# Kernel optimization log

Hardware: AMD Instinct MI355X
Metric: run time of the kernel (lower is better)

## Reference

```python
import jax, jax.numpy as jnp
import numpy as np

PATCH = 16  # patch_size

def _patchify(images, p=PATCH):
    # images: [B, H, W] -> patches: [B, N, p*p] in raster order
    B, H, W = images.shape
    x = images.reshape(B, H // p, p, W // p, p)
    x = x.transpose(0, 1, 3, 2, 4)  # [B, H/p, W/p, p, p]
    return x.reshape(B, (H // p) * (W // p), p * p)

def setup_inputs() -> dict:
    key = jax.random.key(0)
    k1, k2 = jax.random.split(key)
    images = jax.random.normal(k1, (64, 256, 256), dtype=jnp.float32)
    vocab = jax.random.normal(k2, (4096, 256), dtype=jnp.float32)  # [V, patch^2]
    return {"images": images, "vocab": vocab}

def reference(images, vocab):
    # forward_patches: patchify (raster ordering -> identity permutation)
    patches = _patchify(images)  # [B, N, D]
    # forward_tokens: torch.cdist + argmin. argmin of Euclidean distance
    # equals argmin of squared distance; expand ||x-v||^2 to avoid the
    # explicit [B, N, V, D] difference tensor.
    v2 = jnp.sum(vocab * vocab, axis=-1)                      # [V]
    xv = jnp.einsum('bnd,vd->bnv', patches, vocab)            # [B, N, V]
    x2 = jnp.sum(patches * patches, axis=-1, keepdims=True)   # [B, N, 1]
    d2 = x2 - 2.0 * xv + v2                                   # [B, N, V]
    tokens = jnp.argmin(d2, axis=-1)                          # [B, N] int
    return patches, tokens
```

## Files before the change

kernel.cpp:

```cpp
#include <hip/hip_runtime.h>
#include <math.h>

#define PS      16
#define D       256
#define V       4096
#define M       16384
#define NSPLIT  64
#define PAIR_CAP 1048576
#define QMARGIN 130

typedef _Float16 half8 __attribute__((ext_vector_type(8)));
typedef _Float16 half4 __attribute__((ext_vector_type(4)));
typedef float    f32x4 __attribute__((ext_vector_type(4)));

__device__ __forceinline__ void gload_lds16(const void* g, void* l) {
  __builtin_amdgcn_global_load_lds(
      (const __attribute__((address_space(1))) unsigned int*)g,
      (__attribute__((address_space(3))) unsigned int*)l, 16, 0, 0);
}


__global__ __launch_bounds__(256) void prep_kernel(
    const float* __restrict__ img, const float* __restrict__ vocab,
    float* __restrict__ outp, _Float16* __restrict__ Ah2,
    _Float16* __restrict__ Vh2, float* __restrict__ v2,
    int* __restrict__ paircount) {
  if (blockIdx.x < 4096) {
    if (blockIdx.x == 0 && threadIdx.x == 0) *paircount = 0;
    const int t  = blockIdx.x * 256 + threadIdx.x;
    const int o4 = t << 2;
    const int m   = o4 >> 8;
    const int d   = o4 & 255;
    const int b   = m >> 8;
    const int n   = m & 255;
    const int py = n >> 4, px = n & 15, i = d >> 4, j = d & 15;
    const float4 v = *(const float4*)(img + (b << 16) + ((py * PS + i) << 8) + px * PS + j);
    *(float4*)(outp + o4) = v;
    half4 h = { (_Float16)v.x, (_Float16)v.y, (_Float16)v.z, (_Float16)v.w };
    const int fa = (m >> 6) * 16384 + (d >> 5) * 2048 + ((m >> 4) & 3) * 512 +
                   ((d >> 3) & 3) * 128 + (m & 15) * 8 + (d & 7);
    *(half4*)(Ah2 + fa) = h;
  } else {
    const int gtid = (blockIdx.x - 4096) * 256 + threadIdx.x;
    const int c    = gtid >> 6;
    const int lane = gtid & 63;
    const int d0   = lane << 2;
    const float4 v = *(const float4*)(vocab + (size_t)c * D + d0);
    half4 h = { (_Float16)v.x, (_Float16)v.y, (_Float16)v.z, (_Float16)v.w };
    const int fv = (c >> 8) * 65536 + (d0 >> 5) * 8192 + ((c >> 4) & 15) * 512 +
                   ((d0 >> 3) & 3) * 128 + (c & 15) * 8 + (d0 & 7);
    *(half4*)(Vh2 + fv) = h;
    float s = v.x * v.x + v.y * v.y + v.z * v.z + v.w * v.w;
    #pragma unroll
    for (int off = 32; off > 0; off >>= 1) s += __shfl_down(s, off);
    if (lane == 0) v2[c] = s;
  }
}

__global__ __launch_bounds__(256, 4) void gemm_score_kernel(
    const _Float16* __restrict__ Ah2,
    const _Float16* __restrict__ Vh2,
    const float* __restrict__ v2,
    unsigned* __restrict__ pk1, unsigned* __restrict__ pk2) {
  __shared__ __align__(16) _Float16 Af[8 * 64 * 32];

  const int tid  = threadIdx.x;
  const int lane = tid & 63;
  const int wid  = tid >> 6;
  const int rowblk = blockIdx.x;
  const int sp     = blockIdx.y;
  const int row0 = rowblk * 64;
  const int col0 = sp * 256 + wid * 64;
  const int grp  = sp * 4 + wid;

  {
    const _Float16* src = Ah2 + (size_t)rowblk * 16384 + wid * 4096 + lane * 8;
    _Float16* dst = Af + wid * 4096;
    #pragma unroll
    for (int t = 0; t < 8; ++t)
      gload_lds16(src + t * 512, dst + t * 512);
  }
  __syncthreads();

  const int cl = lane & 15;
  const int q  = lane >> 4;
  const _Float16* Ak = Af + q * 128 + cl * 8;
  const _Float16* Bk = Vh2 + (size_t)sp * 65536 + wid * 2048 + q * 128 + cl * 8;

  f32x4 acc[4][4];
  #pragma unroll
  for (int i = 0; i < 4; ++i)
    #pragma unroll
    for (int j = 0; j < 4; ++j) acc[i][j] = (f32x4){0.f, 0.f, 0.f, 0.f};

  #pragma unroll 1
  for (int kt = 0; kt < 8; ++kt) {
    half8 av[4], bp[4];
    #pragma unroll
    for (int i = 0; i < 4; ++i) av[i] = *(const half8*)(Bk + i * 512);
    #pragma unroll
    for (int j = 0; j < 4; ++j) bp[j] = *(const half8*)(Ak + j * 512);
    Bk += 8192; Ak += 2048;
    #pragma unroll
    for (int i = 0; i < 4; ++i)
      #pragma unroll
      for (int j = 0; j < 4; ++j)
        acc[i][j] = __builtin_amdgcn_mfma_f32_16x16x32_f16(av[i], bp[j], acc[i][j], 0, 0, 0);
  }

  float Cv[16];
  #pragma unroll
  for (int i = 0; i < 4; ++i) {
    const float4 vq = *(const float4*)(v2 + col0 + i * 16 + q * 4);
    #pragma unroll
    for (int r = 0; r < 4; ++r) Cv[i * 4 + r] = fmaf(vq[r], 512.0f, 524288.0f);
  }
  #pragma unroll
  for (int j = 0; j < 4; ++j) {
    unsigned K1 = 0xFFFFFFFFu, K2 = 0xFFFFFFFFu;
    #pragma unroll
    for (int i = 0; i < 4; ++i)
      #pragma unroll
      for (int r = 0; r < 4; ++r) {
        const unsigned key =
            ((unsigned)fmaf(-1024.0f, acc[i][j][r], Cv[i * 4 + r]) << 12) |
            (unsigned)(col0 + i * 16 + q * 4 + r);
        K2 = min(K2, max(K1, key));
        K1 = min(K1, key);
      }
    #pragma unroll
    for (int mask = 16; mask <= 32; mask <<= 1) {
      const unsigned o1 = (unsigned)__shfl_xor((int)K1, mask);
      const unsigned o2 = (unsigned)__shfl_xor((int)K2, mask);
      K2 = min(min(K2, o2), max(K1, o1));
      K1 = min(K1, o1);
    }
    if (q == 0) {
      pk1[(size_t)grp * M + row0 + j * 16 + cl] = K1;
      pk2[(size_t)grp * M + row0 + j * 16 + cl] = K2;
    }
  }
}

__global__ __launch_bounds__(256) void reduce_gather_kernel(
    const unsigned* __restrict__ pk1, const unsigned* __restrict__ pk2,
    float* __restrict__ tok, unsigned long long* __restrict__ minkey,
    unsigned* __restrict__ pairs, int* __restrict__ paircount) {
  const int m = blockIdx.x * 256 + threadIdx.x;
  unsigned K1 = 0xFFFFFFFFu, K2 = 0xFFFFFFFFu;
  for (int s = 0; s < NSPLIT; ++s) {
    const unsigned b1 = pk1[(size_t)s * M + m];
    const unsigned b2 = pk2[(size_t)s * M + m];
    K2 = min(min(K2, b2), max(K1, b1));
    K1 = min(K1, b1);
  }
  tok[m] = (float)(K1 & 4095u);
  minkey[m] = 0xFFFFFFFFFFFFFFFFull;
  if ((int)(K2 >> 12) - (int)(K1 >> 12) <= QMARGIN) {
    const int th = (int)(K1 >> 12) + QMARGIN;
    int cnt = 0;
    for (int s = 0; s < NSPLIT; ++s) {
      const unsigned b1 = pk1[(size_t)s * M + m];
      const unsigned b2 = pk2[(size_t)s * M + m];
      cnt += ((int)(b2 >> 12) <= th) ? 64
           : (((int)(b1 >> 12) <= th) ? 1 : 0);
    }
    int base = atomicAdd(paircount, cnt);
    if (base + cnt <= PAIR_CAP) {
      const unsigned mh = (unsigned)m << 12;
      for (int s = 0; s < NSPLIT; ++s) {
        const unsigned b1 = pk1[(size_t)s * M + m];
        const unsigned b2 = pk2[(size_t)s * M + m];
        if ((int)(b2 >> 12) <= th) {
          for (int r = 0; r < 64; ++r) pairs[base + r] = mh | (unsigned)(s * 64 + r);
          base += 64;
        } else if ((int)(b1 >> 12) <= th) {
          pairs[base++] = mh | (b1 & 4095u);
        }
      }
    }
  }
}

__global__ __launch_bounds__(256) void refine_score(
    const float* __restrict__ patches, const float* __restrict__ vocab,
    const unsigned* __restrict__ pairs, const int* __restrict__ paircount,
    unsigned long long* __restrict__ minkey) {
  const int lane = threadIdx.x & 63;
  const int gw = (blockIdx.x * 256 + threadIdx.x) >> 6;
  const int nw = (gridDim.x * 256) >> 6;
  int np = *paircount;
  if (np > PAIR_CAP) np = PAIR_CAP;
  for (int i = gw; i < np; i += nw) {
    const unsigned pr = pairs[i];
    const int m = pr >> 12, row = pr & 4095;
    const float4 pv = *(const float4*)(patches + (size_t)m * D + (lane << 2));
    const float4 vv = *(const float4*)(vocab + (size_t)row * D + (lane << 2));
    double acc = 0.0, df;
    df = (double)pv.x - (double)vv.x; acc = fma(df, df, acc);
    df = (double)pv.y - (double)vv.y; acc = fma(df, df, acc);
    df = (double)pv.z - (double)vv.z; acc = fma(df, df, acc);
    df = (double)pv.w - (double)vv.w; acc = fma(df, df, acc);
    #pragma unroll
    for (int off = 32; off > 0; off >>= 1) acc += __shfl_down(acc, off);
    if (lane == 0) {
      const unsigned long long key =
          ((unsigned long long)__double_as_longlong(acc) & ~0xFFFull) | (unsigned)row;
      atomicMin(&minkey[m], key);
    }
  }
}

__global__ __launch_bounds__(256) void refine_final(
    const unsigned* __restrict__ pairs, const int* __restrict__ paircount,
    const unsigned long long* __restrict__ minkey, float* __restrict__ tok) {
  int np = *paircount;
  if (np > PAIR_CAP) np = PAIR_CAP;
  for (int i = blockIdx.x * 256 + threadIdx.x; i < np; i += gridDim.x * 256) {
    const int m = pairs[i] >> 12;
    tok[m] = (float)(unsigned)(minkey[m] & 4095ull);
  }
}

extern "C" void kernel_launch(void* const* d_in, const int* in_sizes, int n_in,
                              void* d_out, int out_size, void* d_ws, size_t ws_size,
                              hipStream_t stream) {
  const float* images = (const float*)d_in[0];
  const float* vocab  = (const float*)d_in[1];
  float* out     = (float*)d_out;
  float* patches = out;
  float* tokens  = out + (size_t)M * D;

  char* ws = (char*)d_ws;
  _Float16* Ah2      = (_Float16*)(ws);
  _Float16* Vh2      = (_Float16*)(ws + 8388608);
  float*    v2       = (float*)   (ws + 10485760);
  unsigned* pk1      = (unsigned*)(ws + 10502144);
  unsigned* pk2      = (unsigned*)(ws + 14696448);
  unsigned long long* minkey = (unsigned long long*)(ws + 18890752);
  int*      paircount= (int*)     (ws + 19021824);
  unsigned* pairs    = (unsigned*)(ws + 19021888);

  prep_kernel<<<4096 + 1024, 256, 0, stream>>>(images, vocab, patches, Ah2,
                                               Vh2, v2, paircount);
  gemm_score_kernel<<<dim3(M / 64, V / 256), 256, 0, stream>>>(Ah2, Vh2, v2, pk1, pk2);
  reduce_gather_kernel<<<M / 256, 256, 0, stream>>>(pk1, pk2, tokens, minkey,
                                                    pairs, paircount);
  refine_score<<<256, 256, 0, stream>>>(patches, vocab, pairs, paircount, minkey);
  refine_final<<<32, 256, 0, stream>>>(pairs, paircount, minkey, tokens);
}
```

Before: 175.0 us.

## Shrink GEMM column tile, swap grid order, merge wave top-2 in LDS, parallelize reduce

The GEMM block now covers 128 vocab columns (32 per wave) instead of 256, with a grid whose fast axis is the column split. Pairs of waves merge their top-2 keys through LDS before writing, which keeps 64 split groups. Occupancy rises from 4 to 5 blocks per SIMD, and the reduce kernel splits the 64-way scan across 4 waves followed by an LDS merge. Each A tile is loaded from LDS twice as often relative to the compute, and the extra syncs add overhead. The refine kernels also get larger grids.

```diff
diff --git a/kernel.cpp b/kernel.cpp
--- a/kernel.cpp
+++ b/kernel.cpp
@@ -57,7 +57,7 @@
   }
 }
 
-__global__ __launch_bounds__(256, 4) void gemm_score_kernel(
+__global__ __launch_bounds__(256, 5) void gemm_score_kernel(
     const _Float16* __restrict__ Ah2,
     const _Float16* __restrict__ Vh2,
     const float* __restrict__ v2,
@@ -67,11 +67,10 @@
   const int tid  = threadIdx.x;
   const int lane = tid & 63;
   const int wid  = tid >> 6;
-  const int rowblk = blockIdx.x;
-  const int sp     = blockIdx.y;
+  const int sp     = blockIdx.x;
+  const int rowblk = blockIdx.y;
   const int row0 = rowblk * 64;
-  const int col0 = sp * 256 + wid * 64;
-  const int grp  = sp * 4 + wid;
+  const int c0w  = sp * 128 + wid * 32;
 
   {
     const _Float16* src = Ah2 + (size_t)rowblk * 16384 + wid * 4096 + lane * 8;
@@ -85,46 +84,48 @@
   const int cl = lane & 15;
   const int q  = lane >> 4;
   const _Float16* Ak = Af + q * 128 + cl * 8;
-  const _Float16* Bk = Vh2 + (size_t)sp * 65536 + wid * 2048 + q * 128 + cl * 8;
-
-  f32x4 acc[4][4];
+  const _Float16* Bk = Vh2 + (c0w >> 8) * 65536 + ((c0w >> 4) & 15) * 512 +
+                       q * 128 + cl * 8;
+
+  f32x4 acc[2][4];
   #pragma unroll
-  for (int i = 0; i < 4; ++i)
+  for (int i = 0; i < 2; ++i)
     #pragma unroll
     for (int j = 0; j < 4; ++j) acc[i][j] = (f32x4){0.f, 0.f, 0.f, 0.f};
 
   #pragma unroll 1
   for (int kt = 0; kt < 8; ++kt) {
-    half8 av[4], bp[4];
-    #pragma unroll
-    for (int i = 0; i < 4; ++i) av[i] = *(const half8*)(Bk + i * 512);
+    half8 av[2], bp[4];
+    #pragma unroll
+    for (int i = 0; i < 2; ++i) av[i] = *(const half8*)(Bk + i * 512);
     #pragma unroll
     for (int j = 0; j < 4; ++j) bp[j] = *(const half8*)(Ak + j * 512);
     Bk += 8192; Ak += 2048;
     #pragma unroll
-    for (int i = 0; i < 4; ++i)
+    for (int i = 0; i < 2; ++i)
       #pragma unroll
       for (int j = 0; j < 4; ++j)
         acc[i][j] = __builtin_amdgcn_mfma_f32_16x16x32_f16(av[i], bp[j], acc[i][j], 0, 0, 0);
   }
 
-  float Cv[16];
+  float Cv[8];
   #pragma unroll
-  for (int i = 0; i < 4; ++i) {
-    const float4 vq = *(const float4*)(v2 + col0 + i * 16 + q * 4);
+  for (int i = 0; i < 2; ++i) {
+    const float4 vq = *(const float4*)(v2 + c0w + i * 16 + q * 4);
     #pragma unroll
     for (int r = 0; r < 4; ++r) Cv[i * 4 + r] = fmaf(vq[r], 512.0f, 524288.0f);
   }
+  unsigned wk1[4], wk2[4];
   #pragma unroll
   for (int j = 0; j < 4; ++j) {
     unsigned K1 = 0xFFFFFFFFu, K2 = 0xFFFFFFFFu;
     #pragma unroll
-    for (int i = 0; i < 4; ++i)
+    for (int i = 0; i < 2; ++i)
       #pragma unroll
       for (int r = 0; r < 4; ++r) {
         const unsigned key =
             ((unsigned)fmaf(-1024.0f, acc[i][j][r], Cv[i * 4 + r]) << 12) |
-            (unsigned)(col0 + i * 16 + q * 4 + r);
+            (unsigned)(c0w + i * 16 + q * 4 + r);
         K2 = min(K2, max(K1, key));
         K1 = min(K1, key);
       }
@@ -135,10 +136,27 @@
       K2 = min(min(K2, o2), max(K1, o1));
       K1 = min(K1, o1);
     }
-    if (q == 0) {
-      pk1[(size_t)grp * M + row0 + j * 16 + cl] = K1;
-      pk2[(size_t)grp * M + row0 + j * 16 + cl] = K2;
-    }
+    wk1[j] = K1; wk2[j] = K2;
+  }
+  __syncthreads();
+  unsigned* scr = (unsigned*)Af;
+  if (q == 0) {
+    #pragma unroll
+    for (int j = 0; j < 4; ++j) {
+      const int idx = (wid >> 1) * 256 + (wid & 1) * 128 + (j * 16 + cl) * 2;
+      scr[idx] = wk1[j]; scr[idx + 1] = wk2[j];
+    }
+  }
+  __syncthreads();
+  if (tid < 128) {
+    const int pair = tid >> 6, row = tid & 63;
+    const unsigned a1 = scr[pair * 256 + row * 2], a2 = scr[pair * 256 + row * 2 + 1];
+    const unsigned b1 = scr[pair * 256 + 128 + row * 2], b2 = scr[pair * 256 + 128 + row * 2 + 1];
+    const unsigned K2 = min(min(a2, b2), max(a1, b1));
+    const unsigned K1 = min(a1, b1);
+    const int grp = sp * 2 + pair;
+    pk1[(size_t)grp * M + row0 + row] = K1;
+    pk2[(size_t)grp * M + row0 + row] = K2;
   }
 }
 
@@ -146,36 +164,51 @@
     const unsigned* __restrict__ pk1, const unsigned* __restrict__ pk2,
     float* __restrict__ tok, unsigned long long* __restrict__ minkey,
     unsigned* __restrict__ pairs, int* __restrict__ paircount) {
-  const int m = blockIdx.x * 256 + threadIdx.x;
+  __shared__ unsigned r1[4][64], r2[4][64];
+  const int tid = threadIdx.x;
+  const int mo  = tid & 63;
+  const int wid = tid >> 6;
+  const int m = blockIdx.x * 64 + mo;
   unsigned K1 = 0xFFFFFFFFu, K2 = 0xFFFFFFFFu;
-  for (int s = 0; s < NSPLIT; ++s) {
+  for (int s = wid * 16; s < wid * 16 + 16; ++s) {
     const unsigned b1 = pk1[(size_t)s * M + m];
     const unsigned b2 = pk2[(size_t)s * M + m];
     K2 = min(min(K2, b2), max(K1, b1));
     K1 = min(K1, b1);
   }
-  tok[m] = (float)(K1 & 4095u);
-  minkey[m] = 0xFFFFFFFFFFFFFFFFull;
-  if ((int)(K2 >> 12) - (int)(K1 >> 12) <= QMARGIN) {
-    const int th = (int)(K1 >> 12) + QMARGIN;
-    int cnt = 0;
-    for (int s = 0; s < NSPLIT; ++s) {
-      const unsigned b1 = pk1[(size_t)s * M + m];
-      const unsigned b2 = pk2[(size_t)s * M + m];
-      cnt += ((int)(b2 >> 12) <= th) ? 64
-           : (((int)(b1 >> 12) <= th) ? 1 : 0);
-    }
-    int base = atomicAdd(paircount, cnt);
-    if (base + cnt <= PAIR_CAP) {
-      const unsigned mh = (unsigned)m << 12;
+  r1[wid][mo] = K1; r2[wid][mo] = K2;
+  __syncthreads();
+  if (tid < 64) {
+    K1 = 0xFFFFFFFFu; K2 = 0xFFFFFFFFu;
+    #pragma unroll
+    for (int w = 0; w < 4; ++w) {
+      const unsigned b1 = r1[w][mo], b2 = r2[w][mo];
+      K2 = min(min(K2, b2), max(K1, b1));
+      K1 = min(K1, b1);
+    }
+    tok[m] = (float)(K1 & 4095u);
+    minkey[m] = 0xFFFFFFFFFFFFFFFFull;
+    if ((int)(K2 >> 12) - (int)(K1 >> 12) <= QMARGIN) {
+      const int th = (int)(K1 >> 12) + QMARGIN;
+      int cnt = 0;
       for (int s = 0; s < NSPLIT; ++s) {
         const unsigned b1 = pk1[(size_t)s * M + m];
         const unsigned b2 = pk2[(size_t)s * M + m];
-        if ((int)(b2 >> 12) <= th) {
-          for (int r = 0; r < 64; ++r) pairs[base + r] = mh | (unsigned)(s * 64 + r);
-          base += 64;
-        } else if ((int)(b1 >> 12) <= th) {
-          pairs[base++] = mh | (b1 & 4095u);
+        cnt += ((int)(b2 >> 12) <= th) ? 64
+             : (((int)(b1 >> 12) <= th) ? 1 : 0);
+      }
+      int base = atomicAdd(paircount, cnt);
+      if (base + cnt <= PAIR_CAP) {
+        const unsigned mh = (unsigned)m << 12;
+        for (int s = 0; s < NSPLIT; ++s) {
+          const unsigned b1 = pk1[(size_t)s * M + m];
+          const unsigned b2 = pk2[(size_t)s * M + m];
+          if ((int)(b2 >> 12) <= th) {
+            for (int r = 0; r < 64; ++r) pairs[base + r] = mh | (unsigned)(s * 64 + r);
+            base += 64;
+          } else if ((int)(b1 >> 12) <= th) {
+            pairs[base++] = mh | (b1 & 4095u);
+          }
         }
       }
     }
@@ -243,9 +276,9 @@
 
   prep_kernel<<<4096 + 1024, 256, 0, stream>>>(images, vocab, patches, Ah2,
                                                Vh2, v2, paircount);
-  gemm_score_kernel<<<dim3(M / 64, V / 256), 256, 0, stream>>>(Ah2, Vh2, v2, pk1, pk2);
-  reduce_gather_kernel<<<M / 256, 256, 0, stream>>>(pk1, pk2, tokens, minkey,
-                                                    pairs, paircount);
-  refine_score<<<256, 256, 0, stream>>>(patches, vocab, pairs, paircount, minkey);
-  refine_final<<<32, 256, 0, stream>>>(pairs, paircount, minkey, tokens);
-}
+  gemm_score_kernel<<<dim3(V / 128, M / 64), 256, 0, stream>>>(Ah2, Vh2, v2, pk1, pk2);
+  reduce_gather_kernel<<<M / 64, 256, 0, stream>>>(pk1, pk2, tokens, minkey,
+                                                   pairs, paircount);
+  refine_score<<<512, 256, 0, stream>>>(patches, vocab, pairs, paircount, minkey);
+  refine_final<<<64, 256, 0, stream>>>(pairs, paircount, minkey, tokens);
+}
```

After: 159.0 us. -9.1%, faster.
